# Kernel optimization log

Measured on AMD Instinct MI355X. Metric: run time of the kernel, lower is better.

Reference implementation:

```python
import jax, jax.numpy as jnp
from jax import lax
import numpy as np

DIM = 2048
KSZ = 4
BATCH = 4
SEQ = 4096


def setup_inputs() -> dict:
    key = jax.random.key(0)
    k1, k2 = jax.random.split(key)
    x = jax.random.normal(k1, (BATCH, SEQ, DIM), dtype=jnp.float32)
    weight = jax.random.normal(k2, (DIM, 1, KSZ), dtype=jnp.float32) * 0.02
    bias = jnp.zeros((DIM,), dtype=jnp.float32)
    return {"x": x, "weight": weight, "bias": bias}


def reference(x, weight, bias):
    # x: (B, S, D); weight: (D, 1, K) torch layout; bias: (D,)
    K = weight.shape[-1]
    # causal left-pad along sequence
    xp = jnp.pad(x, ((0, 0), (K - 1, 0), (0, 0)))
    # depthwise conv: NWC input, WIO kernel with in-per-group=1, groups=D
    w = jnp.transpose(weight, (2, 1, 0))  # (K, 1, D)
    y = lax.conv_general_dilated(
        xp, w,
        window_strides=(1,),
        padding='VALID',
        dimension_numbers=('NWC', 'WIO', 'NWC'),
        feature_group_count=x.shape[-1],
    )
    return y + bias  # (B, S, D)
```

## Files before the change

### kernel.cpp

```cpp
#include <hip/hip_runtime.h>

#define BB 4
#define SS 4096
#define DD 2048
#define D4 (DD / 4)
#define CHUNK 16
#define NCH (SS / CHUNK)

typedef float v4f __attribute__((ext_vector_type(4)));

__global__ __launch_bounds__(256) void shortconv_kernel(
    const v4f* __restrict__ x,
    const v4f* __restrict__ w4,
    const v4f* __restrict__ bias4,
    v4f* __restrict__ y)
{
    const int t    = blockIdx.x * 256 + threadIdx.x;
    const int d4   = t & (D4 - 1);
    const int rest = t >> 9;
    const int ch   = rest & (NCH - 1);
    const int b    = rest >> 8;

    const size_t base = ((size_t)b * SS + (size_t)(ch * CHUNK)) * D4 + (size_t)d4;

    const v4f wr0 = w4[4 * d4 + 0];
    const v4f wr1 = w4[4 * d4 + 1];
    const v4f wr2 = w4[4 * d4 + 2];
    const v4f wr3 = w4[4 * d4 + 3];
    const v4f bv  = bias4[d4];

    v4f xs[CHUNK + 3];
    if (ch == 0) {
        xs[0] = (v4f)(0.f);
        xs[1] = (v4f)(0.f);
        xs[2] = (v4f)(0.f);
    } else {
        xs[0] = x[base - 3 * (size_t)D4];
        xs[1] = x[base - 2 * (size_t)D4];
        xs[2] = x[base - 1 * (size_t)D4];
    }
#pragma unroll
    for (int i = 0; i < CHUNK; ++i) {
        xs[3 + i] = x[base + (size_t)i * D4];
    }

    __builtin_amdgcn_sched_barrier(0);

#pragma unroll
    for (int i = 0; i < CHUNK; ++i) {
        const v4f x0 = xs[i + 0];
        const v4f x1 = xs[i + 1];
        const v4f x2 = xs[i + 2];
        const v4f x3 = xs[i + 3];
        v4f r;
        r.x = bv.x + wr0.x * x0.x + wr0.y * x1.x + wr0.z * x2.x + wr0.w * x3.x;
        r.y = bv.y + wr1.x * x0.y + wr1.y * x1.y + wr1.z * x2.y + wr1.w * x3.y;
        r.z = bv.z + wr2.x * x0.z + wr2.y * x1.z + wr2.z * x2.z + wr2.w * x3.z;
        r.w = bv.w + wr3.x * x0.w + wr3.y * x1.w + wr3.z * x2.w + wr3.w * x3.w;
        __builtin_nontemporal_store(r, &y[base + (size_t)i * D4]);
    }
}

extern "C" void kernel_launch(void* const* d_in, const int* in_sizes, int n_in,
                              void* d_out, int out_size, void* d_ws, size_t ws_size,
                              hipStream_t stream) {
    const float* x    = (const float*)d_in[0];
    const float* w    = (const float*)d_in[1];
    const float* bias = (const float*)d_in[2];
    float* out        = (float*)d_out;

    const int total_threads = BB * NCH * D4;
    const int block = 256;
    const int grid  = total_threads / block;

    shortconv_kernel<<<grid, block, 0, stream>>>(
        (const v4f*)x, (const v4f*)w, (const v4f*)bias, (v4f*)out);
}
```

Measured before the change: 237.1 us.

## Stream chunk loads with rolling prefetch, double chunk size, swizzle block order

```diff
diff --git a/kernel.cpp b/kernel.cpp
--- a/kernel.cpp
+++ b/kernel.cpp
@@ -4,8 +4,10 @@
 #define SS 4096
 #define DD 2048
 #define D4 (DD / 4)
-#define CHUNK 16
+#define CHUNK 32
 #define NCH (SS / CHUNK)
+#define NBLK (BB * NCH * D4 / 256)
+#define PF 4
 
 typedef float v4f __attribute__((ext_vector_type(4)));
 
@@ -15,13 +17,12 @@
     const v4f* __restrict__ bias4,
     v4f* __restrict__ y)
 {
-    const int t    = blockIdx.x * 256 + threadIdx.x;
+    const int logical = (blockIdx.x & 7) * (NBLK / 8) + (blockIdx.x >> 3);
+    const int t    = logical * 256 + (int)threadIdx.x;
     const int d4   = t & (D4 - 1);
     const int rest = t >> 9;
     const int ch   = rest & (NCH - 1);
-    const int b    = rest >> 8;
-
-    const size_t base = ((size_t)b * SS + (size_t)(ch * CHUNK)) * D4 + (size_t)d4;
+    const int b    = rest >> 7;
 
     const v4f wr0 = w4[4 * d4 + 0];
     const v4f wr1 = w4[4 * d4 + 1];
@@ -29,35 +30,38 @@
     const v4f wr3 = w4[4 * d4 + 3];
     const v4f bv  = bias4[d4];
 
-    v4f xs[CHUNK + 3];
+    const size_t base = ((size_t)b * SS + (size_t)(ch * CHUNK)) * D4 + (size_t)d4;
+
+    v4f h0, h1, h2;
     if (ch == 0) {
-        xs[0] = (v4f)(0.f);
-        xs[1] = (v4f)(0.f);
-        xs[2] = (v4f)(0.f);
+        h0 = (v4f)(0.f);
+        h1 = (v4f)(0.f);
+        h2 = (v4f)(0.f);
     } else {
-        xs[0] = x[base - 3 * (size_t)D4];
-        xs[1] = x[base - 2 * (size_t)D4];
-        xs[2] = x[base - 1 * (size_t)D4];
-    }
-#pragma unroll
-    for (int i = 0; i < CHUNK; ++i) {
-        xs[3 + i] = x[base + (size_t)i * D4];
+        h0 = x[base - 3 * (size_t)D4];
+        h1 = x[base - 2 * (size_t)D4];
+        h2 = x[base - 1 * (size_t)D4];
     }
 
-    __builtin_amdgcn_sched_barrier(0);
+    v4f pf[PF];
+#pragma unroll
+    for (int i = 0; i < PF; ++i) pf[i] = x[base + (size_t)i * D4];
 
 #pragma unroll
     for (int i = 0; i < CHUNK; ++i) {
-        const v4f x0 = xs[i + 0];
-        const v4f x1 = xs[i + 1];
-        const v4f x2 = xs[i + 2];
-        const v4f x3 = xs[i + 3];
+        const v4f x3 = pf[i & (PF - 1)];
+        if (i + PF < CHUNK) {
+            pf[i & (PF - 1)] = x[base + (size_t)(i + PF) * D4];
+        }
         v4f r;
-        r.x = bv.x + wr0.x * x0.x + wr0.y * x1.x + wr0.z * x2.x + wr0.w * x3.x;
-        r.y = bv.y + wr1.x * x0.y + wr1.y * x1.y + wr1.z * x2.y + wr1.w * x3.y;
-        r.z = bv.z + wr2.x * x0.z + wr2.y * x1.z + wr2.z * x2.z + wr2.w * x3.z;
-        r.w = bv.w + wr3.x * x0.w + wr3.y * x1.w + wr3.z * x2.w + wr3.w * x3.w;
+        r.x = bv.x + wr0.x * h0.x + wr0.y * h1.x + wr0.z * h2.x + wr0.w * x3.x;
+        r.y = bv.y + wr1.x * h0.y + wr1.y * h1.y + wr1.z * h2.y + wr1.w * x3.y;
+        r.z = bv.z + wr2.x * h0.z + wr2.y * h1.z + wr2.z * h2.z + wr2.w * x3.z;
+        r.w = bv.w + wr3.x * h0.w + wr3.y * h1.w + wr3.z * h2.w + wr3.w * x3.w;
         __builtin_nontemporal_store(r, &y[base + (size_t)i * D4]);
+        h0 = h1;
+        h1 = h2;
+        h2 = x3;
     }
 }
 
@@ -69,10 +73,6 @@
     const float* bias = (const float*)d_in[2];
     float* out        = (float*)d_out;
 
-    const int total_threads = BB * NCH * D4;
-    const int block = 256;
-    const int grid  = total_threads / block;
-
-    shortconv_kernel<<<grid, block, 0, stream>>>(
+    shortconv_kernel<<<NBLK, 256, 0, stream>>>(
         (const v4f*)x, (const v4f*)w, (const v4f*)bias, (v4f*)out);
 }
```

Result: no change. 236.5 us (-0.3%).
